# Kernel optimization log

Measured on AMD Instinct MI355X. Metric: run time of the kernel, lower is better.

## Reference

```python
import jax, jax.numpy as jnp
import numpy as np

B, N, D, H, PSI = 8, 7225, 256, 8, 64
DH = D // H
DF = 4 * D
EPS = 1e-5


def _ln(x, g, b):
    m = jnp.mean(x, axis=-1, keepdims=True)
    v = jnp.mean((x - m) ** 2, axis=-1, keepdims=True)
    return (x - m) / jnp.sqrt(v + EPS) * g + b


def _gelu(x):
    return jax.nn.gelu(x, approximate=False)


def setup_inputs() -> dict:
    key = jax.random.key(0)
    ks = jax.random.split(key, 16)
    w = lambda k, s: (jax.random.normal(k, s, dtype=jnp.float32) * 0.02)
    inp = {
        'x': jax.random.normal(ks[0], (B, N, D), dtype=jnp.float32),
        'fx': jax.random.normal(ks[1], (B, N, D), dtype=jnp.float32),
        'ln1_g': jnp.ones((D,), jnp.float32), 'ln1_b': jnp.zeros((D,), jnp.float32),
        'Wq': w(ks[2], (D, D)), 'Wk': w(ks[3], (D, D)), 'Wv': w(ks[4], (D, D)),
        'Wo': w(ks[5], (D, D)), 'bo': jnp.zeros((D,), jnp.float32),
        'ln2_g': jnp.ones((D,), jnp.float32), 'ln2_b': jnp.zeros((D,), jnp.float32),
        'mlp_W1': w(ks[6], (D, DF)), 'mlp_b1': jnp.zeros((DF,), jnp.float32),
        'mlp_W2': w(ks[7], (DF, D)), 'mlp_b2': jnp.zeros((D,), jnp.float32),
        'proj_W1': w(ks[8], (D, D)), 'proj_b1': jnp.zeros((D,), jnp.float32),
        'proj_W2': w(ks[9], (D, PSI)), 'proj_b2': jnp.zeros((PSI,), jnp.float32),
        'mu': jnp.zeros((PSI,), jnp.float32),
        'ln3_g': jnp.ones((D,), jnp.float32), 'ln3_b': jnp.zeros((D,), jnp.float32),
        'mlp2_W1': w(ks[10], (D, DF)), 'mlp2_b1': jnp.zeros((DF,), jnp.float32),
        'mlp2_W2': w(ks[11], (DF, D)), 'mlp2_b2': jnp.zeros((D,), jnp.float32),
    }
    return inp


def _forward(x, fx, ln1_g, ln1_b, Wq, Wk, Wv, Wo, bo, ln2_g, ln2_b,
             mlp_W1, mlp_b1, mlp_W2, mlp_b2, proj_W1, proj_b1, proj_W2, proj_b2,
             mu, ln3_g, ln3_b, mlp2_W1, mlp2_b1, mlp2_W2, mlp2_b2):
    # --- linear (kernelized, non-causal) self-attention ---
    h = _ln(x, ln1_g, ln1_b)
    to_heads = lambda t: t.reshape(B, N, H, DH).transpose(0, 2, 1, 3)  # bhnd
    q = to_heads(h @ Wq)
    k = to_heads(h @ Wk)
    v = to_heads(h @ Wv)
    q = jax.nn.softmax(q, axis=-1) * (DH ** -0.5)   # feature-dim softmax
    k = jax.nn.softmax(k, axis=-2)                  # sequence-dim softmax
    ctx = jnp.einsum('bhnd,bhne->bhde', k, v)       # [B,H,DH,DH]
    attn = jnp.einsum('bhnd,bhde->bhne', q, ctx)    # [B,H,N,DH]
    attn = attn.transpose(0, 2, 1, 3).reshape(B, N, D) @ Wo + bo
    x = attn + x

    # --- MLP block (n_layers=0, no residual inside MLP) ---
    h = _ln(x, ln2_g, ln2_b)
    x = _gelu(h @ mlp_W1 + mlp_b1) @ mlp_W2 + mlp_b2 + x

    # --- low-rank projection + covariance whitening (orth=True, training path) ---
    x_ = _gelu(x @ proj_W1 + proj_b1) @ proj_W2 + proj_b2       # [B,N,PSI]
    cov = jnp.einsum('blc,bld->cd', x_, x_) / (B * N)           # [PSI,PSI]
    L = jnp.linalg.cholesky(cov)
    L_inv_T = jnp.linalg.inv(L).T
    x_ = x_ @ L_inv_T

    # --- softplus-scaled low-rank operator on fx ---
    ctx2 = jnp.einsum('blp,bld->bpd', x_, fx)                   # [B,PSI,D]
    fx = jnp.einsum('blp,bpd->bld', x_ * jax.nn.softplus(mu), ctx2)

    fx = _gelu(_ln(fx, ln3_g, ln3_b) @ mlp2_W1 + mlp2_b1) @ mlp2_W2 + mlp2_b2
    return x, fx


def reference(x, fx, ln1_g, ln1_b, Wq, Wk, Wv, Wo, bo, ln2_g, ln2_b,
              mlp_W1, mlp_b1, mlp_W2, mlp_b2, proj_W1, proj_b1, proj_W2, proj_b2,
              mu, ln3_g, ln3_b, mlp2_W1, mlp2_b1, mlp2_W2, mlp2_b2):
    return _forward(x, fx, ln1_g, ln1_b, Wq, Wk, Wv, Wo, bo, ln2_g, ln2_b,
                    mlp_W1, mlp_b1, mlp_W2, mlp_b2, proj_W1, proj_b1, proj_W2, proj_b2,
                    mu, ln3_g, ln3_b, mlp2_W1, mlp2_b1, mlp2_W2, mlp2_b2)
```

## Files before the change

kernel.cpp:

```cpp
#include <hip/hip_runtime.h>
#include <math.h>

typedef unsigned short u16;
typedef unsigned int u32;
typedef float f32x4 __attribute__((ext_vector_type(4)));
typedef __bf16 bf16x8 __attribute__((ext_vector_type(8)));

#define NTOK 57800
#define NSEQ 7225
#define NBATCH 8

static __device__ __forceinline__ float bf2f(u16 u){ u32 x=((u32)u)<<16; float f; __builtin_memcpy(&f,&x,4); return f; }
static __device__ __forceinline__ u16 f2bf(float f){ __bf16 h = (__bf16)f; u16 u; __builtin_memcpy(&u,&h,2); return u; }
static __device__ __forceinline__ float gelu_f(float v){
  float t = v * v;
  float w = fmaf(t, -0.07135481627f, -1.5957691216f);
  float e = __expf(w * v);
  return v * __builtin_amdgcn_rcpf(1.0f + e);
}

static __device__ __forceinline__ void gl16(const u16* g, u16* l){
  __builtin_amdgcn_global_load_lds((const __attribute__((address_space(1))) void*)g,
                                   (__attribute__((address_space(3))) void*)l, 16, 0, 0);
}

static __device__ __forceinline__ float rdlane(float v, int lane){
  int i; __builtin_memcpy(&i,&v,4);
  int r = __builtin_amdgcn_readlane(i, lane);
  float f; __builtin_memcpy(&f,&r,4);
  return f;
}

struct WJobs { const float* src[10]; u16* dst[10]; int K[10]; int N[10]; };
__global__ __launch_bounds__(256) void wtrans_all(WJobs j){
  int z = blockIdx.z;
  int K = j.K[z], N = j.N[z];
  int bk = blockIdx.x*32, bn = blockIdx.y*32;
  if (bk >= K || bn >= N) return;
  const float* src = j.src[z];
  u16* dst = j.dst[z];
  __shared__ float t[32][33];
  int tx = threadIdx.x&31, ty = threadIdx.x>>5;
  #pragma unroll
  for (int u=0;u<4;u++){
    int k = bk+ty+u*8, n = bn+tx;
    if (k<K && n<N) t[ty+u*8][tx] = src[(long)k*N+n];
  }
  __syncthreads();
  #pragma unroll
  for (int u=0;u<4;u++){
    int n = bn+ty+u*8, k = bk+tx;
    if (n<N && k<K) dst[(long)n*K+k] = f2bf(t[tx][ty+u*8]);
  }
}

__global__ __launch_bounds__(256) void ln_kernel(const float* __restrict__ in, const float* __restrict__ g,
                                                 const float* __restrict__ b, u16* __restrict__ out, int rows){
  int wid = threadIdx.x>>6, lane = threadIdx.x&63;
  int row = blockIdx.x*4 + wid;
  if (row >= rows) return;
  const float4 xv = *reinterpret_cast<const float4*>(in + (long)row*256 + lane*4);
  float s = xv.x+xv.y+xv.z+xv.w;
  float s2 = xv.x*xv.x+xv.y*xv.y+xv.z*xv.z+xv.w*xv.w;
  #pragma unroll
  for (int o=32;o;o>>=1){ s += __shfl_xor(s,o,64); s2 += __shfl_xor(s2,o,64); }
  float mean = s*(1.f/256.f);
  float var = fmaxf(s2*(1.f/256.f) - mean*mean, 0.f);
  float rstd = rsqrtf(var + 1e-5f);
  float4 gv = *reinterpret_cast<const float4*>(g + lane*4);
  float4 bv = *reinterpret_cast<const float4*>(b + lane*4);
  ushort4 o4;
  o4.x = f2bf((xv.x-mean)*rstd*gv.x + bv.x);
  o4.y = f2bf((xv.y-mean)*rstd*gv.y + bv.y);
  o4.z = f2bf((xv.z-mean)*rstd*gv.z + bv.z);
  o4.w = f2bf((xv.w-mean)*rstd*gv.w + bv.w);
  *reinterpret_cast<ushort4*>(out + (long)row*256 + lane*4) = o4;
}

template<bool BIASF, bool RESF, bool GELUF, bool OF32, bool OBF16>
__global__ __launch_bounds__(256) void gemm3(const u16* __restrict__ A, const u16* __restrict__ Bt,
    const float* __restrict__ bias, const float* __restrict__ resid,
    float* __restrict__ outF, u16* __restrict__ outB,
    int M, int N, int K, int gn, long aB, long bB, long cB)
{
  __shared__ __align__(16) u16 lds[2][8192];
  int nwg = gridDim.x, bid = blockIdx.x;
  int qx = nwg>>3, rx = nwg&7;
  int xcd = bid&7, lin = bid>>3;
  int swz = (xcd<rx)? (xcd*(qx+1)+lin) : (rx + xcd*qx + lin);
  int mi_ = swz/gn;
  int m0 = mi_*128, n0 = (swz - mi_*gn)*128;

  const u16* Ab  = A  + (long)blockIdx.z*aB;
  const u16* Btb = Bt + (long)blockIdx.z*bB;
  long coff = (long)blockIdx.z*cB;
  int tid = threadIdx.x, w = tid>>6, l = tid&63;
  int lr = l>>3;
  int csrc = (((l&7) ^ lr) << 3);
  int l15 = l&15, lq = l>>4;
  int wm = (w>>1)*64, wn = (w&1)*64;
  int sx = (l15&7)<<3;

  f32x4 acc[4][4];
  #pragma unroll
  for (int a=0;a<4;a++)
    #pragma unroll
    for (int b2=0;b2<4;b2++)
      #pragma unroll
      for (int r2=0;r2<4;r2++) acc[a][b2][r2]=0.f;

  int nt = K>>6;

  auto STAGE = [&](int k0){
    #pragma unroll
    for (int u=0;u<4;u++){
      int rr = w*32 + u*8;
      gl16(Ab  + (long)(m0+rr+lr)*K + k0 + csrc, &lds[0][0] + rr*64 + l*8);
      gl16(Btb + (long)(n0+rr+lr)*K + k0 + csrc, &lds[1][0] + rr*64 + l*8);
    }
  };

  STAGE(0);
  for (int t=0;;t++){
    __syncthreads();
    #pragma unroll
    for (int ks=0;ks<2;ks++){
      bf16x8 af[4], bfv[4];
      int ko = ks*32 + lq*8;
      #pragma unroll
      for (int mi=0;mi<4;mi++)
        af[mi]  = *reinterpret_cast<const bf16x8*>(&lds[0][0] + (wm+mi*16+l15)*64 + (ko ^ sx));
      #pragma unroll
      for (int ni=0;ni<4;ni++)
        bfv[ni] = *reinterpret_cast<const bf16x8*>(&lds[1][0] + (wn+ni*16+l15)*64 + (ko ^ sx));
      #pragma unroll
      for (int mi=0;mi<4;mi++)
        #pragma unroll
        for (int ni=0;ni<4;ni++)
          acc[mi][ni] = __builtin_amdgcn_mfma_f32_16x16x32_bf16(bfv[ni], af[mi], acc[mi][ni], 0,0,0);
    }
    if (t+1 == nt) break;
    __syncthreads();
    STAGE((t+1)<<6);
  }

  #pragma unroll
  for (int mi=0;mi<4;mi++){
    int row = m0 + wm + mi*16 + l15;
    if (row >= M) continue;
    #pragma unroll
    for (int ni=0;ni<4;ni++){
      int col0 = n0 + wn + ni*16 + lq*4;
      if (col0 >= N) continue;
      f32x4 v = acc[mi][ni];
      if (BIASF){
        const float4 bv = *reinterpret_cast<const float4*>(bias + col0);
        v[0]+=bv.x; v[1]+=bv.y; v[2]+=bv.z; v[3]+=bv.w;
      }
      long idx = (long)row*N + col0;
      if (RESF){
        const float4 rv = *reinterpret_cast<const float4*>(resid + coff + idx);
        v[0]+=rv.x; v[1]+=rv.y; v[2]+=rv.z; v[3]+=rv.w;
      }
      if (GELUF){
        #pragma unroll
        for (int r2=0;r2<4;r2++) v[r2] = gelu_f(v[r2]);
      }
      if (OF32){
        float4 o; o.x=v[0]; o.y=v[1]; o.z=v[2]; o.w=v[3];
        *reinterpret_cast<float4*>(outF + coff + idx) = o;
      }
      if (OBF16){
        ushort4 o; o.x=f2bf(v[0]); o.y=f2bf(v[1]); o.z=f2bf(v[2]); o.w=f2bf(v[3]);
        *reinterpret_cast<ushort4*>(outB + coff + idx) = o;
      }
    }
  }
}

__global__ __launch_bounds__(256) void ctx_part(const u16* __restrict__ qkvb, float* __restrict__ part,
                                                float* __restrict__ spart2){
  int ch = blockIdx.x, bh = blockIdx.y; int b = bh>>3, h = bh&7;
  __shared__ float ek[8][32], vl[8][32];
  int tid = threadIdx.x;
  int d = tid&31, eg = (tid>>5)*4;
  float acc[4] = {0.f,0.f,0.f,0.f};
  float ssum = 0.f;
  int n0 = ch*226; int n1 = n0+226; if (n1 > NSEQ) n1 = NSEQ;
  for (int nb=n0; nb<n1; nb+=8){
    #pragma unroll
    for (int u=0;u<2;u++){
      int idx = tid + u*256; int r = idx>>6, c = idx&63;
      int n = nb + r;
      if (c < 32) ek[r][c]    = (n<n1)? __expf(bf2f(qkvb[((long)(b*NSEQ+n))*768 + 256 + h*32 + c])) : 0.f;
      else        vl[r][c-32] = (n<n1)? bf2f(qkvb[((long)(b*NSEQ+n))*768 + 512 + h*32 + (c-32)]) : 0.f;
    }
    __syncthreads();
    #pragma unroll
    for (int r=0;r<8;r++){
      float kv = ek[r][d];
      ssum += kv;
      #pragma unroll
      for (int j=0;j<4;j++) acc[j] += kv * vl[r][eg+j];
    }
    __syncthreads();
  }
  #pragma unroll
  for (int j=0;j<4;j++) part[((long)(bh*32+ch))*1024 + d*32 + eg + j] = acc[j];
  if (tid < 32) spart2[(bh*32+ch)*32 + d] = ssum;
}
__global__ void ctx_red(const float* __restrict__ part, const float* __restrict__ spart2,
                        float* __restrict__ ctx){
  int bh = blockIdx.x;
  __shared__ float sinvl[32];
  int tid = threadIdx.x;
  if (tid < 32){
    float s=0.f;
    for (int ch=0;ch<32;ch++) s += spart2[(bh*32+ch)*32 + tid];
    sinvl[tid] = 1.0f/s;
  }
  __syncthreads();
  for (int idx=tid; idx<1024; idx+=256){
    float s=0.f;
    for (int ch=0;ch<32;ch++) s += part[((long)(bh*32+ch))*1024 + idx];
    ctx[(long)bh*1024 + idx] = s * sinvl[idx>>5];
  }
}

__global__ __launch_bounds__(256) void qsoftmax(const u16* __restrict__ qkvb, u16* __restrict__ qsb){
  int wid = threadIdx.x>>6, lane = threadIdx.x&63;
  int n = blockIdx.x*4 + wid;
  int b = blockIdx.y;
  if (n >= NSEQ) return;
  const ushort4 qv = *reinterpret_cast<const ushort4*>(qkvb + ((long)(b*NSEQ+n))*768 + lane*4);
  float e0 = __expf(bf2f(qv.x)), e1 = __expf(bf2f(qv.y)),
        e2 = __expf(bf2f(qv.z)), e3 = __expf(bf2f(qv.w));
  float s = e0+e1+e2+e3;
  s += __shfl_xor(s,1,64); s += __shfl_xor(s,2,64); s += __shfl_xor(s,4,64);
  float r = 0.17677669529663687f / s;
  ushort4 o; o.x=f2bf(e0*r); o.y=f2bf(e1*r); o.z=f2bf(e2*r); o.w=f2bf(e3*r);
  *reinterpret_cast<ushort4*>(qsb + ((long)(b*NSEQ+n))*256 + lane*4) = o;
}

__global__ __launch_bounds__(256) void ctx_wo(const float* __restrict__ ctx, const u16* __restrict__ wot,
                                              u16* __restrict__ w2bt){
  int jg = blockIdx.x, b = blockIdx.y;
  int j0 = jg*32;
  __shared__ u16 wol[32][256];
  int tid = threadIdx.x;
  {
    int r = tid>>3, c = (tid&7)*32;
    const uint4* src = reinterpret_cast<const uint4*>(wot + (j0+r)*256 + c);
    uint4* dst = reinterpret_cast<uint4*>(&wol[r][c]);
    dst[0]=src[0]; dst[1]=src[1]; dst[2]=src[2]; dst[3]=src[3];
  }
  int h = tid>>5, d = tid&31;
  float creg[32];
  {
    const float4* cp = reinterpret_cast<const float4*>(ctx + (long)(b*8+h)*1024 + d*32);
    #pragma unroll
    for (int u=0;u<8;u++){ float4 v = cp[u]; creg[u*4]=v.x; creg[u*4+1]=v.y; creg[u*4+2]=v.z; creg[u*4+3]=v.w; }
  }
  __syncthreads();
  for (int jj=0;jj<32;jj++){
    const uint4* wp = reinterpret_cast<const uint4*>(&wol[jj][h*32]);
    float acc = 0.f;
    #pragma unroll
    for (int u=0;u<4;u++){
      uint4 wv = wp[u];
      acc += bf2f((u16)(wv.x&0xffffu))*creg[u*8+0] + bf2f((u16)(wv.x>>16))*creg[u*8+1]
           + bf2f((u16)(wv.y&0xffffu))*creg[u*8+2] + bf2f((u16)(wv.y>>16))*creg[u*8+3]
           + bf2f((u16)(wv.z&0xffffu))*creg[u*8+4] + bf2f((u16)(wv.z>>16))*creg[u*8+5]
           + bf2f((u16)(wv.w&0xffffu))*creg[u*8+6] + bf2f((u16)(wv.w>>16))*creg[u*8+7];
    }
    w2bt[((long)b*256 + j0+jj)*256 + tid] = f2bf(acc);
  }
}

__global__ __launch_bounds__(256) void cov_part(const float* __restrict__ xu, float* __restrict__ part){
  int ch = blockIdx.x;
  __shared__ float xl[2][8][64];
  int tid = threadIdx.x;
  int i = tid&63, jg = (tid>>6)*16;
  int lrow = tid>>5, lcol = (tid&31)*2;
  float acc[16];
  #pragma unroll
  for (int j=0;j<16;j++) acc[j]=0.f;
  int n0 = ch*113;
  const int NT = 15;
  float2 xr2;
  auto LOAD = [&](int t){
    int n = n0 + t*8 + lrow;
    if (n < n0+113 && n < NTOK) xr2 = *reinterpret_cast<const float2*>(xu + (long)n*64 + lcol);
    else { xr2.x = 0.f; xr2.y = 0.f; }
  };
  LOAD(0);
  for (int t=0; t<NT; t++){
    int cur = t&1;
    xl[cur][lrow][lcol] = xr2.x; xl[cur][lrow][lcol+1] = xr2.y;
    __syncthreads();
    if (t+1 < NT) LOAD(t+1);
    #pragma unroll
    for (int r=0;r<8;r++){
      float xv = xl[cur][r][i];
      const float4* fb = reinterpret_cast<const float4*>(&xl[cur][r][jg]);
      float4 f0=fb[0], f1=fb[1], f2=fb[2], f3=fb[3];
      acc[0]+=xv*f0.x; acc[1]+=xv*f0.y; acc[2]+=xv*f0.z; acc[3]+=xv*f0.w;
      acc[4]+=xv*f1.x; acc[5]+=xv*f1.y; acc[6]+=xv*f1.z; acc[7]+=xv*f1.w;
      acc[8]+=xv*f2.x; acc[9]+=xv*f2.y; acc[10]+=xv*f2.z; acc[11]+=xv*f2.w;
      acc[12]+=xv*f3.x; acc[13]+=xv*f3.y; acc[14]+=xv*f3.z; acc[15]+=xv*f3.w;
    }
    __syncthreads();
  }
  #pragma unroll
  for (int j=0;j<16;j++) part[(long)ch*4096 + (jg+j)*64 + i] = acc[j];
}
__global__ void cov_red(const float* __restrict__ part, float* __restrict__ cov){
  __shared__ float red[4][64];
  int o = blockIdx.x*64 + (threadIdx.x&63);
  int sl = threadIdx.x>>6;
  float s=0.f;
  for (int ch=sl; ch<512; ch+=4) s += part[(long)ch*4096 + o];
  if (sl>0) red[sl][threadIdx.x&63] = s;
  __syncthreads();
  if (sl==0){
    s += red[1][threadIdx.x&63] + red[2][threadIdx.x&63] + red[3][threadIdx.x&63];
    cov[o] = s * (1.0f/57800.0f);
  }
}

__global__ __launch_bounds__(64) void chol_inv(const float* __restrict__ cov, float* __restrict__ Linv){
  int t = threadIdx.x;
  float r[64];
  #pragma unroll
  for (int k=0;k<16;k++){
    float4 v4 = *reinterpret_cast<const float4*>(cov + (long)t*64 + k*4);
    r[k*4]=v4.x; r[k*4+1]=v4.y; r[k*4+2]=v4.z; r[k*4+3]=v4.w;
  }
  float dinv[64];
  #pragma unroll
  for (int j=0;j<64;j++){
    float ajj = rdlane(r[j], j);
    float ljj = sqrtf(fmaxf(ajj, 1e-20f));
    float rinv = 1.0f / ljj;
    dinv[j] = rinv;
    float ltj = r[j] * rinv;
    r[j] = ltj;
    #pragma unroll
    for (int k=j+1;k<64;k++){
      float lkj = rdlane(ltj, k);
      r[k] -= ltj * lkj;
    }
  }
  float v[64];
  #pragma unroll
  for (int k=0;k<64;k++) v[k] = (k==t) ? 1.f : 0.f;
  #pragma unroll
  for (int i=0;i<64;i++){
    float xi = v[i] * dinv[i];
    Linv[i*64 + t] = xi;
    #pragma unroll
    for (int k=i+1;k<64;k++){
      v[k] -= rdlane(r[i], k) * xi;
    }
  }
}

__global__ __launch_bounds__(256) void whiten(const float* __restrict__ xu, const float* __restrict__ Linv,
                                              const float* __restrict__ mu, u16* __restrict__ xw, u16* __restrict__ xws){
  __shared__ float Ll[64][65];
  int tid = threadIdx.x;
  for (int u=0; u<16; u++){ int idx = u*256+tid; Ll[idx>>6][idx&63] = Linv[idx]; }
  __syncthreads();
  int wid = tid>>6, lane = tid&63;
  float m = mu[lane];
  float sp = (m > 20.f)? m : log1pf(expf(m));
  for (int rr=0; rr<4; rr++){
    int row = blockIdx.x*16 + wid*4 + rr;
    if (row >= NTOK) continue;
    float xj = xu[(long)row*64 + lane];
    float s = 0.f;
    #pragma unroll
    for (int j=0;j<64;j++) s += __shfl(xj, j, 64) * Ll[lane][j];
    xw[(long)row*64+lane]  = f2bf(s);
    xws[(long)row*64+lane] = f2bf(s * sp);
  }
}

__global__ __launch_bounds__(256) void ctx2_part(const u16* __restrict__ xw, const float* __restrict__ fx,
                                                 float* __restrict__ part){
  int cg = blockIdx.x, ch = blockIdx.y, b = blockIdx.z;
  __shared__ float xwlf[2][8][64];
  __shared__ float fxl[2][8][64];
  int tid = threadIdx.x;
  int p = tid&63, jg = (tid>>6)*16;
  int c0 = cg*64;
  int lrow = tid>>5, lcol = (tid&31)*2;
  float acc[16];
  #pragma unroll
  for (int j=0;j<16;j++) acc[j]=0.f;
  int n0 = ch*226;
  const int NT = 29;
  float2 fxr; float xwr0, xwr1;
  auto LOAD = [&](int t){
    int n = n0 + t*8 + lrow;
    if (n < n0+226 && n < NSEQ){
      fxr = *reinterpret_cast<const float2*>(fx + ((long)b*NSEQ+n)*256 + c0 + lcol);
      u32 xv = *reinterpret_cast<const u32*>(xw + ((long)b*NSEQ+n)*64 + lcol);
      xwr0 = bf2f((u16)(xv&0xffffu)); xwr1 = bf2f((u16)(xv>>16));
    } else { fxr.x=0.f; fxr.y=0.f; xwr0=0.f; xwr1=0.f; }
  };
  LOAD(0);
  for (int t=0; t<NT; t++){
    int cur = t&1;
    xwlf[cur][lrow][lcol] = xwr0; xwlf[cur][lrow][lcol+1] = xwr1;
    fxl[cur][lrow][lcol] = fxr.x; fxl[cur][lrow][lcol+1] = fxr.y;
    __syncthreads();
    if (t+1 < NT) LOAD(t+1);
    #pragma unroll
    for (int r=0;r<8;r++){
      float xv = xwlf[cur][r][p];
      const float4* fb = reinterpret_cast<const float4*>(&fxl[cur][r][jg]);
      float4 f0=fb[0], f1=fb[1], f2=fb[2], f3=fb[3];
      acc[0]+=xv*f0.x; acc[1]+=xv*f0.y; acc[2]+=xv*f0.z; acc[3]+=xv*f0.w;
      acc[4]+=xv*f1.x; acc[5]+=xv*f1.y; acc[6]+=xv*f1.z; acc[7]+=xv*f1.w;
      acc[8]+=xv*f2.x; acc[9]+=xv*f2.y; acc[10]+=xv*f2.z; acc[11]+=xv*f2.w;
      acc[12]+=xv*f3.x; acc[13]+=xv*f3.y; acc[14]+=xv*f3.z; acc[15]+=xv*f3.w;
    }
    __syncthreads();
  }
  long base = ((long)(b*32+ch)*256 + c0 + jg)*64 + p;
  #pragma unroll
  for (int j=0;j<16;j++) part[base + (long)j*64] = acc[j];
}
__global__ void ctx2_red(const float* __restrict__ part, u16* __restrict__ c2t){
  int b = blockIdx.y;
  int idx0 = blockIdx.x*1024 + threadIdx.x;
  #pragma unroll
  for (int u=0;u<4;u++){
    int id = idx0 + u*256;
    float s=0.f;
    for (int ch=0;ch<32;ch++) s += part[(long)(b*32+ch)*16384 + id];
    c2t[(long)b*16384 + id] = f2bf(s);
  }
}

extern "C" void kernel_launch(void* const* d_in, const int* in_sizes, int n_in,
                              void* d_out, int out_size, void* d_ws, size_t ws_size,
                              hipStream_t stream)
{
  (void)in_sizes; (void)n_in; (void)out_size; (void)ws_size;
  const float* x     = (const float*)d_in[0];
  const float* fx    = (const float*)d_in[1];
  const float* ln1_g = (const float*)d_in[2];
  const float* ln1_b = (const float*)d_in[3];
  const float* Wq    = (const float*)d_in[4];
  const float* Wk    = (const float*)d_in[5];
  const float* Wv    = (const float*)d_in[6];
  const float* Wo    = (const float*)d_in[7];
  const float* bo    = (const float*)d_in[8];
  const float* ln2_g = (const float*)d_in[9];
  const float* ln2_b = (const float*)d_in[10];
  const float* mW1   = (const float*)d_in[11];
  const float* mb1   = (const float*)d_in[12];
  const float* mW2   = (const float*)d_in[13];
  const float* mb2   = (const float*)d_in[14];
  const float* pW1   = (const float*)d_in[15];
  const float* pb1   = (const float*)d_in[16];
  const float* pW2   = (const float*)d_in[17];
  const float* pb2   = (const float*)d_in[18];
  const float* mu    = (const float*)d_in[19];
  const float* ln3_g = (const float*)d_in[20];
  const float* ln3_b = (const float*)d_in[21];
  const float* m2W1  = (const float*)d_in[22];
  const float* m2b1  = (const float*)d_in[23];
  const float* m2W2  = (const float*)d_in[24];
  const float* m2b2  = (const float*)d_in[25];

  char* wsb = (char*)d_ws;
  u16* wt    = (u16*)wsb;
  u16* WQKVT = wt + 0;
  u16* WOT   = wt + 196608;
  u16* W1T   = wt + 262144;
  u16* W2T   = wt + 524288;
  u16* PW1T  = wt + 786432;
  u16* PW2T  = wt + 851968;
  u16* M2W1T = wt + 884736;
  u16* M2W2T = wt + 1146880;

  constexpr size_t OFF_H      = 2818048;
  constexpr size_t OFF_QKV    = 32440320;
  constexpr size_t OFF_ATT    = 150929408;
  constexpr size_t OFF_SPART2 = 180551680;
  constexpr size_t OFF_XU     = 180813824;
  constexpr size_t OFF_CTXP   = OFF_XU;
  constexpr size_t OFF_CTX    = OFF_XU + 8388608;
  constexpr size_t OFF_XW     = 195624960;
  constexpr size_t OFF_XWS    = 203023360;
  constexpr size_t OFF_W2BT   = 210430976;
  constexpr size_t OFF_COVP   = OFF_H;
  constexpr size_t OFF_COV    = OFF_H + 8388608;
  constexpr size_t OFF_LINV   = OFF_H + 8404992;
  constexpr size_t OFF_C2P    = OFF_QKV;
  constexpr size_t OFF_C2T    = OFF_QKV + 16777216;

  u16* h     = (u16*)(wsb + OFF_H);
  u16* qkvb  = (u16*)(wsb + OFF_QKV);
  u16* m1    = qkvb;
  u16* attb  = (u16*)(wsb + OFF_ATT);
  u16* qsb   = (u16*)(wsb + OFF_ATT);
  float* spart2= (float*)(wsb + OFF_SPART2);
  float* ctxp  = (float*)(wsb + OFF_CTXP);
  float* ctxb  = (float*)(wsb + OFF_CTX);
  float* xu    = (float*)(wsb + OFF_XU);
  u16*  xwb    = (u16*)(wsb + OFF_XW);
  u16*  xwsb   = (u16*)(wsb + OFF_XWS);
  float* covp  = (float*)(wsb + OFF_COVP);
  float* cov   = (float*)(wsb + OFF_COV);
  float* Linv  = (float*)(wsb + OFF_LINV);
  float* c2p   = (float*)(wsb + OFF_C2P);
  u16*  c2t    = (u16*)(wsb + OFF_C2T);
  u16*  w2bt   = (u16*)(wsb + OFF_W2BT);

  float* outx  = (float*)d_out;
  float* outfx = outx + 14796800;

  WJobs wj;
  wj.src[0]=Wq;   wj.dst[0]=WQKVT;          wj.K[0]=256;  wj.N[0]=256;
  wj.src[1]=Wk;   wj.dst[1]=WQKVT+65536;    wj.K[1]=256;  wj.N[1]=256;
  wj.src[2]=Wv;   wj.dst[2]=WQKVT+131072;   wj.K[2]=256;  wj.N[2]=256;
  wj.src[3]=Wo;   wj.dst[3]=WOT;            wj.K[3]=256;  wj.N[3]=256;
  wj.src[4]=mW1;  wj.dst[4]=W1T;            wj.K[4]=256;  wj.N[4]=1024;
  wj.src[5]=mW2;  wj.dst[5]=W2T;            wj.K[5]=1024; wj.N[5]=256;
  wj.src[6]=pW1;  wj.dst[6]=PW1T;           wj.K[6]=256;  wj.N[6]=256;
  wj.src[7]=pW2;  wj.dst[7]=PW2T;           wj.K[7]=256;  wj.N[7]=64;
  wj.src[8]=m2W1; wj.dst[8]=M2W1T;          wj.K[8]=256;  wj.N[8]=1024;
  wj.src[9]=m2W2; wj.dst[9]=M2W2T;          wj.K[9]=1024; wj.N[9]=256;
  wtrans_all<<<dim3(32,32,10),256,0,stream>>>(wj);

  ln_kernel<<<14450,256,0,stream>>>(x, ln1_g, ln1_b, h, NTOK);
  gemm3<false,false,false,false,true><<<dim3(452*6,1,1),256,0,stream>>>(
      h, WQKVT, nullptr, nullptr, nullptr, qkvb, NTOK, 768, 256, 6, 0,0,0);
  qsoftmax<<<dim3(1807,8),256,0,stream>>>(qkvb, qsb);
  ctx_part<<<dim3(32,64),256,0,stream>>>(qkvb, ctxp, spart2);
  ctx_red<<<64,256,0,stream>>>(ctxp, spart2, ctxb);
  ctx_wo<<<dim3(8,8),256,0,stream>>>(ctxb, WOT, w2bt);
  gemm3<true,true,false,true,false><<<dim3(57*2,1,8),256,0,stream>>>(
      qsb, w2bt, bo, x, outx, nullptr, NSEQ, 256, 256, 2,
      (long)NSEQ*256, 256*256, (long)NSEQ*256);

  ln_kernel<<<14450,256,0,stream>>>(outx, ln2_g, ln2_b, h, NTOK);
  gemm3<true,false,true,false,true><<<dim3(452*8,1,1),256,0,stream>>>(
      h, W1T, mb1, nullptr, nullptr, m1, NTOK, 1024, 256, 8, 0,0,0);
  gemm3<true,true,false,true,true><<<dim3(452*2,1,1),256,0,stream>>>(
      m1, W2T, mb2, outx, outx, attb, NTOK, 256, 1024, 2, 0,0,0);

  gemm3<true,false,true,false,true><<<dim3(452*2,1,1),256,0,stream>>>(
      attb, PW1T, pb1, nullptr, nullptr, h, NTOK, 256, 256, 2, 0,0,0);
  gemm3<true,false,false,true,false><<<dim3(452,1,1),256,0,stream>>>(
      h, PW2T, pb2, nullptr, xu, nullptr, NTOK, 64, 256, 1, 0,0,0);

  cov_part<<<512,256,0,stream>>>(xu, covp);
  cov_red<<<64,256,0,stream>>>(covp, cov);
  chol_inv<<<1,64,0,stream>>>(cov, Linv);
  whiten<<<3613,256,0,stream>>>(xu, Linv, mu, xwb, xwsb);

  ctx2_part<<<dim3(4,32,8),256,0,stream>>>(xwb, fx, c2p);
  ctx2_red<<<dim3(16,8),256,0,stream>>>(c2p, c2t);
  gemm3<false,false,false,true,false><<<dim3(57*2,1,8),256,0,stream>>>(
      xwsb, c2t, nullptr, nullptr, outfx, nullptr, NSEQ, 256, 64, 2,
      (long)NSEQ*64, 256*64, (long)NSEQ*256);

  ln_kernel<<<14450,256,0,stream>>>(outfx, ln3_g, ln3_b, h, NTOK);
  gemm3<true,false,true,false,true><<<dim3(452*8,1,1),256,0,stream>>>(
      h, M2W1T, m2b1, nullptr, nullptr, m1, NTOK, 1024, 256, 8, 0,0,0);
  gemm3<true,false,false,true,false><<<dim3(452*2,1,1),256,0,stream>>>(
      m1, M2W2T, m2b2, nullptr, outfx, nullptr, NTOK, 256, 1024, 2, 0,0,0);
}
```

Baseline: 821.0 us.

## Double-buffer GEMM LDS stages and widen ctx2_part to all channels per block

The shared GEMM kernel now keeps two LDS buffers, so the async global-to-LDS load of the next K tile is issued before the MFMAs on the current tile, with one barrier per iteration instead of two. This is meant to hide load latency behind compute, at the cost of doubling LDS per block (64 KB), which may lower occupancy. Separately, ctx2_part has each block handle all 256 fx columns with 64 accumulators per thread rather than splitting columns across 4 blocks. That reuses each xw load across all columns, but it cuts the grid to 256 blocks and raises register pressure.

```diff
diff --git a/kernel.cpp b/kernel.cpp
--- a/kernel.cpp
+++ b/kernel.cpp
@@ -83,7 +83,7 @@
     float* __restrict__ outF, u16* __restrict__ outB,
     int M, int N, int K, int gn, long aB, long bB, long cB)
 {
-  __shared__ __align__(16) u16 lds[2][8192];
+  __shared__ __align__(16) u16 lds[2][2][8192];
   int nwg = gridDim.x, bid = blockIdx.x;
   int qx = nwg>>3, rx = nwg&7;
   int xcd = bid&7, lin = bid>>3;
@@ -111,37 +111,39 @@
 
   int nt = K>>6;
 
-  auto STAGE = [&](int k0){
+  auto STAGE = [&](int k0, int bufi){
     #pragma unroll
     for (int u=0;u<4;u++){
       int rr = w*32 + u*8;
-      gl16(Ab  + (long)(m0+rr+lr)*K + k0 + csrc, &lds[0][0] + rr*64 + l*8);
-      gl16(Btb + (long)(n0+rr+lr)*K + k0 + csrc, &lds[1][0] + rr*64 + l*8);
+      gl16(Ab  + (long)(m0+rr+lr)*K + k0 + csrc, &lds[bufi][0][0] + rr*64 + l*8);
+      gl16(Btb + (long)(n0+rr+lr)*K + k0 + csrc, &lds[bufi][1][0] + rr*64 + l*8);
     }
   };
 
-  STAGE(0);
-  for (int t=0;;t++){
-    __syncthreads();
+  STAGE(0, 0);
+  for (int t=0; t<nt; t++){
+    int cur = t&1;
+    asm volatile("s_waitcnt vmcnt(0)" ::: "memory");
+    __builtin_amdgcn_s_barrier();
+    asm volatile("" ::: "memory");
+    if (t+1 < nt) STAGE((t+1)<<6, cur^1);
+    asm volatile("" ::: "memory");
     #pragma unroll
     for (int ks=0;ks<2;ks++){
       bf16x8 af[4], bfv[4];
       int ko = ks*32 + lq*8;
       #pragma unroll
       for (int mi=0;mi<4;mi++)
-        af[mi]  = *reinterpret_cast<const bf16x8*>(&lds[0][0] + (wm+mi*16+l15)*64 + (ko ^ sx));
+        af[mi]  = *reinterpret_cast<const bf16x8*>(&lds[cur][0][0] + (wm+mi*16+l15)*64 + (ko ^ sx));
       #pragma unroll
       for (int ni=0;ni<4;ni++)
-        bfv[ni] = *reinterpret_cast<const bf16x8*>(&lds[1][0] + (wn+ni*16+l15)*64 + (ko ^ sx));
+        bfv[ni] = *reinterpret_cast<const bf16x8*>(&lds[cur][1][0] + (wn+ni*16+l15)*64 + (ko ^ sx));
       #pragma unroll
       for (int mi=0;mi<4;mi++)
         #pragma unroll
         for (int ni=0;ni<4;ni++)
           acc[mi][ni] = __builtin_amdgcn_mfma_f32_16x16x32_bf16(bfv[ni], af[mi], acc[mi][ni], 0,0,0);
     }
-    if (t+1 == nt) break;
-    __syncthreads();
-    STAGE((t+1)<<6);
   }
 
   #pragma unroll
@@ -389,49 +391,55 @@
 
 __global__ __launch_bounds__(256) void ctx2_part(const u16* __restrict__ xw, const float* __restrict__ fx,
                                                  float* __restrict__ part){
-  int cg = blockIdx.x, ch = blockIdx.y, b = blockIdx.z;
+  int ch = blockIdx.x, b = blockIdx.y;
   __shared__ float xwlf[2][8][64];
-  __shared__ float fxl[2][8][64];
+  __shared__ float fxl[2][8][256];
   int tid = threadIdx.x;
-  int p = tid&63, jg = (tid>>6)*16;
-  int c0 = cg*64;
-  int lrow = tid>>5, lcol = (tid&31)*2;
-  float acc[16];
-  #pragma unroll
-  for (int j=0;j<16;j++) acc[j]=0.f;
+  int p = tid&63, jg = (tid>>6)*64;
+  int lrow = tid>>5, lcol = (tid&31)*8, xcol = (tid&31)*2;
+  float acc[64];
+  #pragma unroll
+  for (int j=0;j<64;j++) acc[j]=0.f;
   int n0 = ch*226;
+  int n1 = n0+226; if (n1 > NSEQ) n1 = NSEQ;
   const int NT = 29;
-  float2 fxr; float xwr0, xwr1;
+  float4 fra, frb; u32 xr;
   auto LOAD = [&](int t){
     int n = n0 + t*8 + lrow;
-    if (n < n0+226 && n < NSEQ){
-      fxr = *reinterpret_cast<const float2*>(fx + ((long)b*NSEQ+n)*256 + c0 + lcol);
-      u32 xv = *reinterpret_cast<const u32*>(xw + ((long)b*NSEQ+n)*64 + lcol);
-      xwr0 = bf2f((u16)(xv&0xffffu)); xwr1 = bf2f((u16)(xv>>16));
-    } else { fxr.x=0.f; fxr.y=0.f; xwr0=0.f; xwr1=0.f; }
+    if (n < n1){
+      const float4* fp = reinterpret_cast<const float4*>(fx + ((long)b*NSEQ+n)*256 + lcol);
+      fra = fp[0]; frb = fp[1];
+      xr = *reinterpret_cast<const u32*>(xw + ((long)b*NSEQ+n)*64 + xcol);
+    } else {
+      fra.x=0.f; fra.y=0.f; fra.z=0.f; fra.w=0.f;
+      frb.x=0.f; frb.y=0.f; frb.z=0.f; frb.w=0.f;
+      xr = 0;
+    }
   };
   LOAD(0);
   for (int t=0; t<NT; t++){
     int cur = t&1;
-    xwlf[cur][lrow][lcol] = xwr0; xwlf[cur][lrow][lcol+1] = xwr1;
-    fxl[cur][lrow][lcol] = fxr.x; fxl[cur][lrow][lcol+1] = fxr.y;
+    xwlf[cur][lrow][xcol]   = bf2f((u16)(xr&0xffffu));
+    xwlf[cur][lrow][xcol+1] = bf2f((u16)(xr>>16));
+    *reinterpret_cast<float4*>(&fxl[cur][lrow][lcol])   = fra;
+    *reinterpret_cast<float4*>(&fxl[cur][lrow][lcol+4]) = frb;
     __syncthreads();
     if (t+1 < NT) LOAD(t+1);
     #pragma unroll
     for (int r=0;r<8;r++){
       float xv = xwlf[cur][r][p];
       const float4* fb = reinterpret_cast<const float4*>(&fxl[cur][r][jg]);
-      float4 f0=fb[0], f1=fb[1], f2=fb[2], f3=fb[3];
-      acc[0]+=xv*f0.x; acc[1]+=xv*f0.y; acc[2]+=xv*f0.z; acc[3]+=xv*f0.w;
-      acc[4]+=xv*f1.x; acc[5]+=xv*f1.y; acc[6]+=xv*f1.z; acc[7]+=xv*f1.w;
-      acc[8]+=xv*f2.x; acc[9]+=xv*f2.y; acc[10]+=xv*f2.z; acc[11]+=xv*f2.w;
-      acc[12]+=xv*f3.x; acc[13]+=xv*f3.y; acc[14]+=xv*f3.z; acc[15]+=xv*f3.w;
+      #pragma unroll
+      for (int c4=0;c4<16;c4++){
+        float4 f = fb[c4];
+        acc[c4*4+0]+=xv*f.x; acc[c4*4+1]+=xv*f.y; acc[c4*4+2]+=xv*f.z; acc[c4*4+3]+=xv*f.w;
+      }
     }
     __syncthreads();
   }
-  long base = ((long)(b*32+ch)*256 + c0 + jg)*64 + p;
-  #pragma unroll
-  for (int j=0;j<16;j++) part[base + (long)j*64] = acc[j];
+  long base = ((long)(b*32+ch)*256 + jg)*64 + p;
+  #pragma unroll
+  for (int j=0;j<64;j++) part[base + (long)j*64] = acc[j];
 }
 __global__ void ctx2_red(const float* __restrict__ part, u16* __restrict__ c2t){
   int b = blockIdx.y;
@@ -565,7 +573,7 @@
   chol_inv<<<1,64,0,stream>>>(cov, Linv);
   whiten<<<3613,256,0,stream>>>(xu, Linv, mu, xwb, xwsb);
 
-  ctx2_part<<<dim3(4,32,8),256,0,stream>>>(xwb, fx, c2p);
+  ctx2_part<<<dim3(32,8),256,0,stream>>>(xwb, fx, c2p);
   ctx2_red<<<dim3(16,8),256,0,stream>>>(c2p, c2t);
   gemm3<false,false,false,true,false><<<dim3(57*2,1,8),256,0,stream>>>(
       xwsb, c2t, nullptr, nullptr, outfx, nullptr, NSEQ, 256, 64, 2,
```

Result: no change. 830.0 us (+1.1%).
